# Performance work log

Hardware: AMD Instinct MI355X
Metric: run time of the kernel (lower is better)

Reference implementation:

```python
import jax, jax.numpy as jnp
import numpy as np

B, L, S, H, E, D = 2, 2048, 2048, 16, 64, 64


def setup_inputs() -> dict:
    key = jax.random.key(0)
    kq, kk, kv = jax.random.split(key, 3)
    queries = jax.random.normal(kq, (B, L, H, E), dtype=jnp.float32)
    keys = jax.random.normal(kk, (B, S, H, E), dtype=jnp.float32)
    values = jax.random.normal(kv, (B, S, H, D), dtype=jnp.float32)
    # causal mask: True = masked out (matches masked_fill semantics)
    causal = jnp.triu(jnp.ones((L, S), dtype=bool), k=1)
    attn_mask = jnp.broadcast_to(causal, (B, L, S))
    return {"queries": queries, "keys": keys, "values": values, "attn_mask": attn_mask}


def reference(queries, keys, values, attn_mask):
    # queries: [B,L,H,E], keys: [B,S,H,E], values: [B,S,H,D], attn_mask: [B,L,S] bool
    E_ = queries.shape[-1]
    scale = 1.0 / jnp.sqrt(jnp.asarray(E_, dtype=queries.dtype))
    scores = jnp.einsum('blhe,bshe->bhls', queries, keys)  # [B,H,L,S]
    scores = jnp.where(attn_mask[:, None, :, :], -jnp.inf, scores)
    A = jax.nn.softmax(scale * scores, axis=-1)
    A = jnp.nan_to_num(A)  # fully-masked rows -> 0 (dropout prob is 0.0)
    V = jnp.einsum('bhls,bshd->blhd', A, values)  # [B,L,H,D]
    return (V, A)
```

## Files before the change

kernel.cpp:

```cpp
#include <hip/hip_runtime.h>
#include <cstdint>
#include <cstddef>

#define B_ 2
#define L_ 2048
#define S_ 2048
#define H_ 16
#define E_ 64
#define D_ 64

#define LOG2E_SCALE 0.18033688011112042f

typedef __attribute__((ext_vector_type(8))) short short8;
typedef __attribute__((ext_vector_type(4))) float float4v;
typedef __attribute__((ext_vector_type(4))) unsigned short ushort4v;
typedef __attribute__((ext_vector_type(2))) unsigned int uint2v;

__device__ __forceinline__ unsigned short f2bf(float f) {
  unsigned u = __builtin_bit_cast(unsigned, f);
  u += 0x7FFFu + ((u >> 16) & 1u);
  return (unsigned short)(u >> 16);
}

__device__ __forceinline__ float myexp2(float x) {
#if __has_builtin(__builtin_amdgcn_exp2f)
  return __builtin_amdgcn_exp2f(x);
#else
  return exp2f(x);
#endif
}

__global__ __launch_bounds__(256)
void conv_nh_kernel(const float* __restrict__ in, unsigned short* __restrict__ out) {
  unsigned idx4 = blockIdx.x * 256u + threadIdx.x;
  unsigned e4 = idx4 & 15u;
  unsigned h  = (idx4 >> 4) & 15u;
  unsigned n  = (idx4 >> 8) & 2047u;
  unsigned b  = idx4 >> 19;
  float4v v = *(const float4v*)(in + (size_t)idx4 * 4u);
  ushort4v o;
  o.x = f2bf(v.x); o.y = f2bf(v.y); o.z = f2bf(v.z); o.w = f2bf(v.w);
  *(ushort4v*)(out + (((size_t)(b * H_ + h) * 2048u + n) * 16u + e4) * 4u) = o;
}

__global__ __launch_bounds__(256)
void conv_vt_kernel(const float* __restrict__ V, unsigned short* __restrict__ VT) {
  __shared__ float tile[64 * 65];
  const int st = blockIdx.x, h = blockIdx.y, b = blockIdx.z;
  const int tid = threadIdx.x;
  const float* vb = V + ((size_t)(b * S_ + st * 64) * H_ + h) * D_;
  #pragma unroll
  for (int i = 0; i < 4; ++i) {
    int e = tid + i * 256;
    int row = e >> 4, c4 = (e & 15) * 4;
    float4v v = *(const float4v*)(vb + (size_t)row * (H_ * D_) + c4);
    tile[row * 65 + c4 + 0] = v.x; tile[row * 65 + c4 + 1] = v.y;
    tile[row * 65 + c4 + 2] = v.z; tile[row * 65 + c4 + 3] = v.w;
  }
  __syncthreads();
  #pragma unroll
  for (int i = 0; i < 4; ++i) {
    int e = tid + i * 256;
    int d = e >> 4, c4 = (e & 15) * 4;
    ushort4v o;
    o.x = f2bf(tile[(c4 + 0) * 65 + d]); o.y = f2bf(tile[(c4 + 1) * 65 + d]);
    o.z = f2bf(tile[(c4 + 2) * 65 + d]); o.w = f2bf(tile[(c4 + 3) * 65 + d]);
    *(ushort4v*)(VT + ((size_t)(b * H_ + h) * D_ + d) * S_ + st * 64 + c4) = o;
  }
}

__global__ __launch_bounds__(256, 4)
void fullattn5_kernel(const unsigned short* __restrict__ Qbf,
                      const unsigned short* __restrict__ Kbf,
                      const unsigned short* __restrict__ VT,
                      float* __restrict__ OutV, float* __restrict__ OutA) {
  __shared__ alignas(16) char smem[18688];
  unsigned short* Ps = (unsigned short*)smem;
  float* Lbuf = (float*)(smem + 18432);
  float* Obuf = (float*)smem;

  const int tid = threadIdx.x;
  const int w = tid >> 6;
  const int lane = tid & 63;
  const int quad = lane >> 4;
  const int n16 = lane & 15;

  const int st = (int)(gridDim.x - 1u - blockIdx.x);
  const int h = blockIdx.y, b = blockIdx.z;
  const int l0 = st * 16;
  const int jt = st >> 2;
  const int doff = (st & 3) * 16;

  float* arow0 = OutA + ((size_t)((b * H_ + h) * L_) + l0) * (size_t)S_;

  {
    const int c4start = (jt + 1) * 16;
    #pragma unroll
    for (int i = 0; i < 4; ++i) {
      float4v* rp = (float4v*)(arow0 + (size_t)(w * 4 + i) * S_);
      for (int c4 = c4start + lane; c4 < S_ / 4; c4 += 64) {
        float4v z = {0.f, 0.f, 0.f, 0.f};
        __builtin_nontemporal_store(z, rp + c4);
      }
    }
  }

  const unsigned short* qrow = Qbf + ((size_t)(b * H_ + h) * L_ + l0 + n16) * E_;
  const short8 qB0 = *(const short8*)(qrow + quad * 8);
  const short8 qB1 = *(const short8*)(qrow + 32 + quad * 8);

  const unsigned short* kbase = Kbf + (size_t)(b * H_ + h) * S_ * E_;
  const unsigned short* vbase = VT + (size_t)(b * H_ + h) * D_ * S_;

  float lsum = 0.f;

  short8 kA0[4], kA1[4], kB0[4], kB1[4];
  auto loadK = [&](int j, short8 (&b0)[4], short8 (&b1)[4]) {
    const unsigned short* kb = kbase + (size_t)j * 64 * E_;
    #pragma unroll
    for (int t = 0; t < 4; ++t) {
      const unsigned short* kr = kb + (size_t)(t * 16 + n16) * E_;
      b0[t] = *(const short8*)(kr + quad * 8);
      b1[t] = *(const short8*)(kr + 32 + quad * 8);
    }
  };

  auto procK = [&](const short8 (&b0)[4], const short8 (&b1)[4], int j) {
    #pragma unroll
    for (int t = 0; t < 4; ++t) {
      float4v acc = {0.f, 0.f, 0.f, 0.f};
      acc = __builtin_amdgcn_mfma_f32_16x16x32_bf16(b0[t], qB0, acc, 0, 0, 0);
      acc = __builtin_amdgcn_mfma_f32_16x16x32_bf16(b1[t], qB1, acc, 0, 0, 0);
      #pragma unroll
      for (int r = 0; r < 4; ++r) {
        float x = acc[r] * LOG2E_SCALE;
        if (j == jt && (t * 16 + quad * 4 + r > doff + n16)) x = -__builtin_inff();
        lsum += myexp2(x);
      }
    }
  };

  if (w <= jt) {
    loadK(w, kA0, kA1);
    int j = w;
    for (;;) {
      if (j + 4 <= jt) loadK(j + 4, kB0, kB1);
      procK(kA0, kA1, j);
      j += 4;
      if (j > jt) break;
      if (j + 4 <= jt) loadK(j + 4, kA0, kA1);
      procK(kB0, kB1, j);
      j += 4;
      if (j > jt) break;
    }
  }

  lsum += __shfl_xor(lsum, 16);
  lsum += __shfl_xor(lsum, 32);
  if (quad == 0) Lbuf[w * 16 + n16] = lsum;
  __syncthreads();
  const float inv_l = 1.0f / (Lbuf[n16] + Lbuf[16 + n16] + Lbuf[32 + n16] + Lbuf[48 + n16]);

  float4v oacc[4];
  #pragma unroll
  for (int t2 = 0; t2 < 4; ++t2) oacc[t2] = (float4v){0.f, 0.f, 0.f, 0.f};

  float* arowL = arow0 + (size_t)n16 * S_ + quad * 4;

  int par = 0;
  for (int j = w; j <= jt; j += 4, par ^= 1) {
    short8 v0f[4], v1f[4];
    #pragma unroll
    for (int t2 = 0; t2 < 4; ++t2) {
      const unsigned short* vr = vbase + (size_t)(t2 * 16 + n16) * S_ + j * 64;
      v0f[t2] = *(const short8*)(vr + quad * 8);
      v1f[t2] = *(const short8*)(vr + 32 + quad * 8);
    }

    const unsigned short* kb = kbase + (size_t)j * 64 * E_;
    unsigned short* psw = Ps + (size_t)((w << 1) | par) * (16 * 72);
    #pragma unroll
    for (int t = 0; t < 4; ++t) {
      const unsigned short* kr = kb + (size_t)(t * 16 + n16) * E_;
      const short8 b0 = *(const short8*)(kr + quad * 8);
      const short8 b1 = *(const short8*)(kr + 32 + quad * 8);
      float4v acc = {0.f, 0.f, 0.f, 0.f};
      acc = __builtin_amdgcn_mfma_f32_16x16x32_bf16(b0, qB0, acc, 0, 0, 0);
      acc = __builtin_amdgcn_mfma_f32_16x16x32_bf16(b1, qB1, acc, 0, 0, 0);
      float p[4];
      #pragma unroll
      for (int r = 0; r < 4; ++r) {
        p[r] = myexp2(acc[r] * LOG2E_SCALE) * inv_l;
        if (j == jt && (t * 16 + quad * 4 + r > doff + n16)) p[r] = 0.f;
      }
      float4v p4 = {p[0], p[1], p[2], p[3]};
      __builtin_nontemporal_store(p4, (float4v*)(arowL + j * 64 + t * 16));
      uint2v dw;
      dw.x = (unsigned)f2bf(p[0]) | ((unsigned)f2bf(p[1]) << 16);
      dw.y = (unsigned)f2bf(p[2]) | ((unsigned)f2bf(p[3]) << 16);
      *(uint2v*)&psw[n16 * 72 + t * 16 + quad * 4] = dw;
    }
    __builtin_amdgcn_wave_barrier();
    const short8 aP0 = *(const short8*)&psw[n16 * 72 + quad * 8];
    const short8 aP1 = *(const short8*)&psw[n16 * 72 + 32 + quad * 8];
    #pragma unroll
    for (int t2 = 0; t2 < 4; ++t2) {
      oacc[t2] = __builtin_amdgcn_mfma_f32_16x16x32_bf16(aP0, v0f[t2], oacc[t2], 0, 0, 0);
      oacc[t2] = __builtin_amdgcn_mfma_f32_16x16x32_bf16(aP1, v1f[t2], oacc[t2], 0, 0, 0);
    }
  }

  __syncthreads();
  #pragma unroll
  for (int t2 = 0; t2 < 4; ++t2)
    #pragma unroll
    for (int r = 0; r < 4; ++r)
      Obuf[(size_t)(w * 16 + quad * 4 + r) * 68 + t2 * 16 + n16] = oacc[t2][r];
  __syncthreads();
  {
    const int row = tid >> 4;
    const int c0 = (tid & 15) * 4;
    float4v s = *(const float4v*)&Obuf[(size_t)row * 68 + c0];
    #pragma unroll
    for (int ww = 1; ww < 4; ++ww) {
      float4v t = *(const float4v*)&Obuf[(size_t)(ww * 16 + row) * 68 + c0];
      s.x += t.x; s.y += t.y; s.z += t.z; s.w += t.w;
    }
    float* op = OutV + ((size_t)(b * L_ + l0 + row) * H_ + h) * D_ + c0;
    __builtin_nontemporal_store(s, (float4v*)op);
  }
}

__global__ __launch_bounds__(256, 4)
void fullattn_fb_kernel(const float* __restrict__ Q, const float* __restrict__ K,
                        const float* __restrict__ V, float* __restrict__ OutV,
                        float* __restrict__ OutA) {
  __shared__ alignas(16) unsigned short Qs[64 * 72];
  __shared__ alignas(16) unsigned short Ks[64 * 72];
  __shared__ alignas(16) unsigned short VTs[64 * 72];
  __shared__ alignas(16) unsigned short Ps[64 * 72];
  const int tid = threadIdx.x;
  const int w = tid >> 6, lane = tid & 63, quad = lane >> 4, n16 = lane & 15;
  const int lt = (int)(gridDim.x - 1u - blockIdx.x);
  const int h = blockIdx.y, b = blockIdx.z;
  const int l0 = lt * 64;
  float* arow0 = OutA + ((size_t)((b * H_ + h) * L_) + l0) * (size_t)S_;
  {
    const int c4start = (lt + 1) * 16;
    for (int rr = w; rr < 64; rr += 4) {
      float4v* rp = (float4v*)(arow0 + (size_t)rr * S_);
      for (int c4 = c4start + lane; c4 < S_ / 4; c4 += 64) {
        float4v z = {0.f, 0.f, 0.f, 0.f};
        __builtin_nontemporal_store(z, rp + c4);
      }
    }
  }
  {
    const float* qb = Q + ((size_t)(b * L_ + l0) * H_ + h) * E_;
    #pragma unroll
    for (int i = 0; i < 4; ++i) {
      int e = tid + i * 256;
      int row = e >> 4, c4 = (e & 15) * 4;
      float4v qv = *(const float4v*)(qb + (size_t)row * (H_ * E_) + c4);
      ushort4v o; o.x = f2bf(qv.x); o.y = f2bf(qv.y); o.z = f2bf(qv.z); o.w = f2bf(qv.w);
      *(ushort4v*)&Qs[row * 72 + c4] = o;
    }
  }
  auto stageK = [&](int j) {
    const float* kb = K + ((size_t)(b * S_ + j * 64) * H_ + h) * E_;
    #pragma unroll
    for (int i = 0; i < 4; ++i) {
      int e = tid + i * 256;
      int row = e >> 4, c4 = (e & 15) * 4;
      float4v kv = *(const float4v*)(kb + (size_t)row * (H_ * E_) + c4);
      ushort4v o; o.x = f2bf(kv.x); o.y = f2bf(kv.y); o.z = f2bf(kv.z); o.w = f2bf(kv.w);
      *(ushort4v*)&Ks[row * 72 + c4] = o;
    }
  };
  auto stageV = [&](int j) {
    const float* vb = V + ((size_t)(b * S_ + j * 64) * H_ + h) * D_;
    const int d = lane;
    #pragma unroll
    for (int i = 0; i < 8; ++i) {
      int s2 = w * 8 + i;
      float f0 = vb[(size_t)(2 * s2) * (H_ * D_) + d];
      float f1 = vb[(size_t)(2 * s2 + 1) * (H_ * D_) + d];
      unsigned pk = (unsigned)f2bf(f0) | ((unsigned)f2bf(f1) << 16);
      *(unsigned*)&VTs[d * 72 + 2 * s2] = pk;
    }
  };
  __syncthreads();
  const short8 aQ0 = *(const short8*)&Qs[(w * 16 + n16) * 72 + quad * 8];
  const short8 aQ1 = *(const short8*)&Qs[(w * 16 + n16) * 72 + 32 + quad * 8];
  float m2[4], lsum[4];
  #pragma unroll
  for (int r = 0; r < 4; ++r) { m2[r] = -__builtin_inff(); lsum[r] = 0.f; }
  for (int j = 0; j <= lt; ++j) {
    stageK(j);
    __syncthreads();
    float x[4][4];
    #pragma unroll
    for (int t = 0; t < 4; ++t) {
      const short8 b0 = *(const short8*)&Ks[(t * 16 + n16) * 72 + quad * 8];
      const short8 b1 = *(const short8*)&Ks[(t * 16 + n16) * 72 + 32 + quad * 8];
      float4v acc = {0.f, 0.f, 0.f, 0.f};
      acc = __builtin_amdgcn_mfma_f32_16x16x32_bf16(aQ0, b0, acc, 0, 0, 0);
      acc = __builtin_amdgcn_mfma_f32_16x16x32_bf16(aQ1, b1, acc, 0, 0, 0);
      #pragma unroll
      for (int r = 0; r < 4; ++r) x[t][r] = acc[r] * LOG2E_SCALE;
    }
    if (j == lt) {
      #pragma unroll
      for (int t = 0; t < 4; ++t)
        #pragma unroll
        for (int r = 0; r < 4; ++r)
          if (t * 16 + n16 > w * 16 + quad * 4 + r) x[t][r] = -__builtin_inff();
    }
    #pragma unroll
    for (int r = 0; r < 4; ++r) {
      float mx = fmaxf(fmaxf(x[0][r], x[1][r]), fmaxf(x[2][r], x[3][r]));
      #pragma unroll
      for (int off = 8; off >= 1; off >>= 1) mx = fmaxf(mx, __shfl_xor(mx, off));
      float mnew = fmaxf(m2[r], mx);
      float alpha = myexp2(m2[r] - mnew);
      float sm = myexp2(x[0][r] - mnew) + myexp2(x[1][r] - mnew) +
                 myexp2(x[2][r] - mnew) + myexp2(x[3][r] - mnew);
      #pragma unroll
      for (int off = 8; off >= 1; off >>= 1) sm += __shfl_xor(sm, off);
      lsum[r] = lsum[r] * alpha + sm;
      m2[r] = mnew;
    }
    __syncthreads();
  }
  float inv_l[4];
  #pragma unroll
  for (int r = 0; r < 4; ++r) inv_l[r] = 1.0f / lsum[r];
  float4v oacc[4];
  #pragma unroll
  for (int t2 = 0; t2 < 4; ++t2) oacc[t2] = (float4v){0.f, 0.f, 0.f, 0.f};
  for (int j = 0; j <= lt; ++j) {
    stageK(j);
    stageV(j);
    __syncthreads();
    float* arow = arow0 + (size_t)(w * 16 + quad * 4) * S_ + j * 64 + n16;
    #pragma unroll
    for (int t = 0; t < 4; ++t) {
      const short8 b0 = *(const short8*)&Ks[(t * 16 + n16) * 72 + quad * 8];
      const short8 b1 = *(const short8*)&Ks[(t * 16 + n16) * 72 + 32 + quad * 8];
      float4v acc = {0.f, 0.f, 0.f, 0.f};
      acc = __builtin_amdgcn_mfma_f32_16x16x32_bf16(aQ0, b0, acc, 0, 0, 0);
      acc = __builtin_amdgcn_mfma_f32_16x16x32_bf16(aQ1, b1, acc, 0, 0, 0);
      #pragma unroll
      for (int r = 0; r < 4; ++r) {
        float p = myexp2(acc[r] * LOG2E_SCALE - m2[r]) * inv_l[r];
        if (j == lt && (t * 16 + n16 > w * 16 + quad * 4 + r)) p = 0.f;
        __builtin_nontemporal_store(p, arow + (size_t)r * S_ + t * 16);
        float pp = __shfl_xor(p, 1);
        unsigned short sp = f2bf(p), spp = f2bf(pp);
        unsigned dw = (n16 & 1) ? ((unsigned)spp | ((unsigned)sp << 16))
                                : ((unsigned)sp | ((unsigned)spp << 16));
        *(unsigned*)&Ps[(w * 16 + quad * 4 + r) * 72 + (t * 16 + (n16 & ~1))] = dw;
      }
    }
    __builtin_amdgcn_wave_barrier();
    const short8 aP0 = *(const short8*)&Ps[(w * 16 + n16) * 72 + quad * 8];
    const short8 aP1 = *(const short8*)&Ps[(w * 16 + n16) * 72 + 32 + quad * 8];
    #pragma unroll
    for (int t2 = 0; t2 < 4; ++t2) {
      const short8 v0 = *(const short8*)&VTs[(t2 * 16 + n16) * 72 + quad * 8];
      const short8 v1 = *(const short8*)&VTs[(t2 * 16 + n16) * 72 + 32 + quad * 8];
      oacc[t2] = __builtin_amdgcn_mfma_f32_16x16x32_bf16(aP0, v0, oacc[t2], 0, 0, 0);
      oacc[t2] = __builtin_amdgcn_mfma_f32_16x16x32_bf16(aP1, v1, oacc[t2], 0, 0, 0);
    }
    __syncthreads();
  }
  float* ob = OutV + ((size_t)(b * L_ + l0 + w * 16 + quad * 4) * H_ + h) * D_ + n16;
  #pragma unroll
  for (int t2 = 0; t2 < 4; ++t2)
    #pragma unroll
    for (int r = 0; r < 4; ++r)
      __builtin_nontemporal_store(oacc[t2][r], ob + (size_t)r * (H_ * D_) + t2 * 16);
}

extern "C" void kernel_launch(void* const* d_in, const int* in_sizes, int n_in,
                              void* d_out, int out_size, void* d_ws, size_t ws_size,
                              hipStream_t stream) {
  (void)in_sizes; (void)n_in; (void)out_size;
  const float* Q = (const float*)d_in[0];
  const float* K = (const float*)d_in[1];
  const float* V = (const float*)d_in[2];
  float* OutV = (float*)d_out;
  float* OutA = (float*)d_out + (size_t)B_ * L_ * H_ * D_;

  const size_t bytes_each = (size_t)B_ * H_ * 2048 * 64 * sizeof(unsigned short);
  if (ws_size >= 3 * bytes_each) {
    unsigned short* Qbf = (unsigned short*)d_ws;
    unsigned short* Kbf = (unsigned short*)((char*)d_ws + bytes_each);
    unsigned short* VTb = (unsigned short*)((char*)d_ws + 2 * bytes_each);
    const int nblk = (B_ * 2048 * H_ * E_ / 4) / 256;
    conv_nh_kernel<<<nblk, 256, 0, stream>>>(Q, Qbf);
    conv_nh_kernel<<<nblk, 256, 0, stream>>>(K, Kbf);
    conv_vt_kernel<<<dim3(S_ / 64, H_, B_), 256, 0, stream>>>(V, VTb);
    fullattn5_kernel<<<dim3(L_ / 16, H_, B_), 256, 0, stream>>>(Qbf, Kbf, VTb, OutV, OutA);
  } else {
    fullattn_fb_kernel<<<dim3(L_ / 64, H_, B_), 256, 0, stream>>>(Q, K, V, OutV, OutA);
  }
}
```

Baseline: 745.5 us.

## Software-pipeline PV pass across key tiles and merge Q/K conversion launches

The second attention pass is restructured so that the PV MFMAs for the previous tile are issued after loading the next K tile, and the V loads for the current tile come after them, overlapping global loads with matrix work. Probability stores to the A output are deferred until after the LDS round-trip. The separate Q and K bf16 conversion launches are merged into one kernel that picks its source by block parity, saving one launch. The pipelining adds register pressure under the 4-blocks-per-SM launch bound and may cause spills.

```diff
diff --git a/kernel.cpp b/kernel.cpp
--- a/kernel.cpp
+++ b/kernel.cpp
@@ -31,8 +31,12 @@
 }
 
 __global__ __launch_bounds__(256)
-void conv_nh_kernel(const float* __restrict__ in, unsigned short* __restrict__ out) {
-  unsigned idx4 = blockIdx.x * 256u + threadIdx.x;
+void conv_qk_kernel(const float* __restrict__ Qi, const float* __restrict__ Ki,
+                    unsigned short* __restrict__ Qo, unsigned short* __restrict__ Ko) {
+  const unsigned bx = blockIdx.x;
+  const float* in = (bx & 1u) ? Ki : Qi;
+  unsigned short* out = (bx & 1u) ? Ko : Qo;
+  unsigned idx4 = (bx >> 1) * 256u + threadIdx.x;
   unsigned e4 = idx4 & 15u;
   unsigned h  = (idx4 >> 4) & 15u;
   unsigned n  = (idx4 >> 8) & 2047u;
@@ -70,7 +74,7 @@
 }
 
 __global__ __launch_bounds__(256, 4)
-void fullattn5_kernel(const unsigned short* __restrict__ Qbf,
+void fullattn6_kernel(const unsigned short* __restrict__ Qbf,
                       const unsigned short* __restrict__ Kbf,
                       const unsigned short* __restrict__ VT,
                       float* __restrict__ OutV, float* __restrict__ OutA) {
@@ -113,45 +117,44 @@
   const unsigned short* vbase = VT + (size_t)(b * H_ + h) * D_ * S_;
 
   float lsum = 0.f;
-
-  short8 kA0[4], kA1[4], kB0[4], kB1[4];
-  auto loadK = [&](int j, short8 (&b0)[4], short8 (&b1)[4]) {
-    const unsigned short* kb = kbase + (size_t)j * 64 * E_;
-    #pragma unroll
-    for (int t = 0; t < 4; ++t) {
-      const unsigned short* kr = kb + (size_t)(t * 16 + n16) * E_;
-      b0[t] = *(const short8*)(kr + quad * 8);
-      b1[t] = *(const short8*)(kr + 32 + quad * 8);
-    }
-  };
-
-  auto procK = [&](const short8 (&b0)[4], const short8 (&b1)[4], int j) {
-    #pragma unroll
-    for (int t = 0; t < 4; ++t) {
-      float4v acc = {0.f, 0.f, 0.f, 0.f};
-      acc = __builtin_amdgcn_mfma_f32_16x16x32_bf16(b0[t], qB0, acc, 0, 0, 0);
-      acc = __builtin_amdgcn_mfma_f32_16x16x32_bf16(b1[t], qB1, acc, 0, 0, 0);
-      #pragma unroll
-      for (int r = 0; r < 4; ++r) {
-        float x = acc[r] * LOG2E_SCALE;
-        if (j == jt && (t * 16 + quad * 4 + r > doff + n16)) x = -__builtin_inff();
-        lsum += myexp2(x);
-      }
-    }
-  };
-
-  if (w <= jt) {
-    loadK(w, kA0, kA1);
-    int j = w;
-    for (;;) {
-      if (j + 4 <= jt) loadK(j + 4, kB0, kB1);
-      procK(kA0, kA1, j);
-      j += 4;
-      if (j > jt) break;
-      if (j + 4 <= jt) loadK(j + 4, kA0, kA1);
-      procK(kB0, kB1, j);
-      j += 4;
-      if (j > jt) break;
+  {
+    short8 kA0[4], kA1[4], kB0[4], kB1[4];
+    auto loadK = [&](int j, short8 (&b0)[4], short8 (&b1)[4]) {
+      const unsigned short* kb = kbase + (size_t)j * 64 * E_;
+      #pragma unroll
+      for (int t = 0; t < 4; ++t) {
+        const unsigned short* kr = kb + (size_t)(t * 16 + n16) * E_;
+        b0[t] = *(const short8*)(kr + quad * 8);
+        b1[t] = *(const short8*)(kr + 32 + quad * 8);
+      }
+    };
+    auto procK = [&](const short8 (&b0)[4], const short8 (&b1)[4], int j) {
+      #pragma unroll
+      for (int t = 0; t < 4; ++t) {
+        float4v acc = {0.f, 0.f, 0.f, 0.f};
+        acc = __builtin_amdgcn_mfma_f32_16x16x32_bf16(b0[t], qB0, acc, 0, 0, 0);
+        acc = __builtin_amdgcn_mfma_f32_16x16x32_bf16(b1[t], qB1, acc, 0, 0, 0);
+        #pragma unroll
+        for (int r = 0; r < 4; ++r) {
+          float x = acc[r] * LOG2E_SCALE;
+          if (j == jt && (t * 16 + quad * 4 + r > doff + n16)) x = -__builtin_inff();
+          lsum += myexp2(x);
+        }
+      }
+    };
+    if (w <= jt) {
+      loadK(w, kA0, kA1);
+      int j = w;
+      for (;;) {
+        if (j + 4 <= jt) loadK(j + 4, kB0, kB1);
+        procK(kA0, kA1, j);
+        j += 4;
+        if (j > jt) break;
+        if (j + 4 <= jt) loadK(j + 4, kA0, kA1);
+        procK(kB0, kB1, j);
+        j += 4;
+        if (j > jt) break;
+      }
     }
   }
 
@@ -167,47 +170,74 @@
 
   float* arowL = arow0 + (size_t)n16 * S_ + quad * 4;
 
-  int par = 0;
-  for (int j = w; j <= jt; j += 4, par ^= 1) {
-    short8 v0f[4], v1f[4];
+  short8 kc0[4], kc1[4];
+  short8 vf0[4], vf1[4];
+  short8 aP0, aP1;
+
+  auto loadK2 = [&](int j) {
+    const unsigned short* kb = kbase + (size_t)j * 64 * E_;
+    #pragma unroll
+    for (int t = 0; t < 4; ++t) {
+      const unsigned short* kr = kb + (size_t)(t * 16 + n16) * E_;
+      kc0[t] = *(const short8*)(kr + quad * 8);
+      kc1[t] = *(const short8*)(kr + 32 + quad * 8);
+    }
+  };
+  auto loadV2 = [&](int j) {
     #pragma unroll
     for (int t2 = 0; t2 < 4; ++t2) {
       const unsigned short* vr = vbase + (size_t)(t2 * 16 + n16) * S_ + j * 64;
-      v0f[t2] = *(const short8*)(vr + quad * 8);
-      v1f[t2] = *(const short8*)(vr + 32 + quad * 8);
-    }
-
-    const unsigned short* kb = kbase + (size_t)j * 64 * E_;
+      vf0[t2] = *(const short8*)(vr + quad * 8);
+      vf1[t2] = *(const short8*)(vr + 32 + quad * 8);
+    }
+  };
+  auto tailQK = [&](int j, int par) {
     unsigned short* psw = Ps + (size_t)((w << 1) | par) * (16 * 72);
+    float4v p4[4];
     #pragma unroll
     for (int t = 0; t < 4; ++t) {
-      const unsigned short* kr = kb + (size_t)(t * 16 + n16) * E_;
-      const short8 b0 = *(const short8*)(kr + quad * 8);
-      const short8 b1 = *(const short8*)(kr + 32 + quad * 8);
       float4v acc = {0.f, 0.f, 0.f, 0.f};
-      acc = __builtin_amdgcn_mfma_f32_16x16x32_bf16(b0, qB0, acc, 0, 0, 0);
-      acc = __builtin_amdgcn_mfma_f32_16x16x32_bf16(b1, qB1, acc, 0, 0, 0);
-      float p[4];
+      acc = __builtin_amdgcn_mfma_f32_16x16x32_bf16(kc0[t], qB0, acc, 0, 0, 0);
+      acc = __builtin_amdgcn_mfma_f32_16x16x32_bf16(kc1[t], qB1, acc, 0, 0, 0);
       #pragma unroll
       for (int r = 0; r < 4; ++r) {
-        p[r] = myexp2(acc[r] * LOG2E_SCALE) * inv_l;
-        if (j == jt && (t * 16 + quad * 4 + r > doff + n16)) p[r] = 0.f;
-      }
-      float4v p4 = {p[0], p[1], p[2], p[3]};
-      __builtin_nontemporal_store(p4, (float4v*)(arowL + j * 64 + t * 16));
+        float p = myexp2(acc[r] * LOG2E_SCALE) * inv_l;
+        if (j == jt && (t * 16 + quad * 4 + r > doff + n16)) p = 0.f;
+        p4[t][r] = p;
+      }
       uint2v dw;
-      dw.x = (unsigned)f2bf(p[0]) | ((unsigned)f2bf(p[1]) << 16);
-      dw.y = (unsigned)f2bf(p[2]) | ((unsigned)f2bf(p[3]) << 16);
+      dw.x = (unsigned)f2bf(p4[t][0]) | ((unsigned)f2bf(p4[t][1]) << 16);
+      dw.y = (unsigned)f2bf(p4[t][2]) | ((unsigned)f2bf(p4[t][3]) << 16);
       *(uint2v*)&psw[n16 * 72 + t * 16 + quad * 4] = dw;
     }
     __builtin_amdgcn_wave_barrier();
-    const short8 aP0 = *(const short8*)&psw[n16 * 72 + quad * 8];
-    const short8 aP1 = *(const short8*)&psw[n16 * 72 + 32 + quad * 8];
+    aP0 = *(const short8*)&psw[n16 * 72 + quad * 8];
+    aP1 = *(const short8*)&psw[n16 * 72 + 32 + quad * 8];
+    __builtin_amdgcn_wave_barrier();
+    #pragma unroll
+    for (int t = 0; t < 4; ++t)
+      __builtin_nontemporal_store(p4[t], (float4v*)(arowL + j * 64 + t * 16));
+  };
+  auto doPV = [&]() {
     #pragma unroll
     for (int t2 = 0; t2 < 4; ++t2) {
-      oacc[t2] = __builtin_amdgcn_mfma_f32_16x16x32_bf16(aP0, v0f[t2], oacc[t2], 0, 0, 0);
-      oacc[t2] = __builtin_amdgcn_mfma_f32_16x16x32_bf16(aP1, v1f[t2], oacc[t2], 0, 0, 0);
-    }
+      oacc[t2] = __builtin_amdgcn_mfma_f32_16x16x32_bf16(aP0, vf0[t2], oacc[t2], 0, 0, 0);
+      oacc[t2] = __builtin_amdgcn_mfma_f32_16x16x32_bf16(aP1, vf1[t2], oacc[t2], 0, 0, 0);
+    }
+  };
+
+  if (w <= jt) {
+    loadK2(w);
+    loadV2(w);
+    tailQK(w, 0);
+    int par = 1;
+    for (int j = w + 4; j <= jt; j += 4, par ^= 1) {
+      loadK2(j);
+      doPV();
+      loadV2(j);
+      tailQK(j, par);
+    }
+    doPV();
   }
 
   __syncthreads();
@@ -398,10 +428,9 @@
     unsigned short* Kbf = (unsigned short*)((char*)d_ws + bytes_each);
     unsigned short* VTb = (unsigned short*)((char*)d_ws + 2 * bytes_each);
     const int nblk = (B_ * 2048 * H_ * E_ / 4) / 256;
-    conv_nh_kernel<<<nblk, 256, 0, stream>>>(Q, Qbf);
-    conv_nh_kernel<<<nblk, 256, 0, stream>>>(K, Kbf);
+    conv_qk_kernel<<<2 * nblk, 256, 0, stream>>>(Q, K, Qbf, Kbf);
     conv_vt_kernel<<<dim3(S_ / 64, H_, B_), 256, 0, stream>>>(V, VTb);
-    fullattn5_kernel<<<dim3(L_ / 16, H_, B_), 256, 0, stream>>>(Qbf, Kbf, VTb, OutV, OutA);
+    fullattn6_kernel<<<dim3(L_ / 16, H_, B_), 256, 0, stream>>>(Qbf, Kbf, VTb, OutV, OutA);
   } else {
     fullattn_fb_kernel<<<dim3(L_ / 64, H_, B_), 256, 0, stream>>>(Q, K, V, OutV, OutA);
   }
```

After: 757.1 us. No clear change (+1.6%).

## Pair complementary causal row tiles per block and merge Q/K conversion launches

Applied to the files above, without the earlier changes.

Each attention block now handles two 16-row query tiles, st and 127-st, so every block does roughly the same amount of causal work. The grid shrinks from 128 to 64 tiles per head, which removes the tail imbalance of the descending-work schedule. The Q and K bf16 conversions are merged into one launch to save a kernel launch. The cost is fewer blocks in flight, serialized passes with extra syncthreads inside each block, and a slightly larger LDS footprint.

```diff
diff --git a/kernel.cpp b/kernel.cpp
--- a/kernel.cpp
+++ b/kernel.cpp
@@ -31,8 +31,12 @@
 }
 
 __global__ __launch_bounds__(256)
-void conv_nh_kernel(const float* __restrict__ in, unsigned short* __restrict__ out) {
-  unsigned idx4 = blockIdx.x * 256u + threadIdx.x;
+void conv_qk_kernel(const float* __restrict__ Qi, const float* __restrict__ Ki,
+                    unsigned short* __restrict__ Qo, unsigned short* __restrict__ Ko) {
+  const unsigned bx = blockIdx.x;
+  const float* in = (bx & 1u) ? Ki : Qi;
+  unsigned short* out = (bx & 1u) ? Ko : Qo;
+  unsigned idx4 = (bx >> 1) * 256u + threadIdx.x;
   unsigned e4 = idx4 & 15u;
   unsigned h  = (idx4 >> 4) & 15u;
   unsigned n  = (idx4 >> 8) & 2047u;
@@ -70,11 +74,11 @@
 }
 
 __global__ __launch_bounds__(256, 4)
-void fullattn5_kernel(const unsigned short* __restrict__ Qbf,
+void fullattn7_kernel(const unsigned short* __restrict__ Qbf,
                       const unsigned short* __restrict__ Kbf,
                       const unsigned short* __restrict__ VT,
                       float* __restrict__ OutV, float* __restrict__ OutA) {
-  __shared__ alignas(16) char smem[18688];
+  __shared__ alignas(16) char smem[18944];
   unsigned short* Ps = (unsigned short*)smem;
   float* Lbuf = (float*)(smem + 18432);
   float* Obuf = (float*)smem;
@@ -85,15 +89,19 @@
   const int quad = lane >> 4;
   const int n16 = lane & 15;
 
-  const int st = (int)(gridDim.x - 1u - blockIdx.x);
   const int h = blockIdx.y, b = blockIdx.z;
-  const int l0 = st * 16;
-  const int jt = st >> 2;
-  const int doff = (st & 3) * 16;
-
-  float* arow0 = OutA + ((size_t)((b * H_ + h) * L_) + l0) * (size_t)S_;
-
-  {
+  const int stA = (int)blockIdx.x;
+  const int stB = 127 - stA;
+  const int jtA = stA >> 2, doffA = (stA & 3) * 16;
+  const int jtB = stB >> 2, doffB = (stB & 3) * 16;
+
+  const unsigned short* kbase = Kbf + (size_t)(b * H_ + h) * S_ * E_;
+  const unsigned short* vbase = VT + (size_t)(b * H_ + h) * D_ * S_;
+
+  float* arowA = OutA + ((size_t)((b * H_ + h) * L_) + stA * 16) * (size_t)S_;
+  float* arowB = OutA + ((size_t)((b * H_ + h) * L_) + stB * 16) * (size_t)S_;
+
+  auto zfill = [&](float* arow0, int jt) {
     const int c4start = (jt + 1) * 16;
     #pragma unroll
     for (int i = 0; i < 4; ++i) {
@@ -103,121 +111,123 @@
         __builtin_nontemporal_store(z, rp + c4);
       }
     }
-  }
-
-  const unsigned short* qrow = Qbf + ((size_t)(b * H_ + h) * L_ + l0 + n16) * E_;
-  const short8 qB0 = *(const short8*)(qrow + quad * 8);
-  const short8 qB1 = *(const short8*)(qrow + 32 + quad * 8);
-
-  const unsigned short* kbase = Kbf + (size_t)(b * H_ + h) * S_ * E_;
-  const unsigned short* vbase = VT + (size_t)(b * H_ + h) * D_ * S_;
-
-  float lsum = 0.f;
-
-  short8 kA0[4], kA1[4], kB0[4], kB1[4];
-  auto loadK = [&](int j, short8 (&b0)[4], short8 (&b1)[4]) {
-    const unsigned short* kb = kbase + (size_t)j * 64 * E_;
-    #pragma unroll
-    for (int t = 0; t < 4; ++t) {
-      const unsigned short* kr = kb + (size_t)(t * 16 + n16) * E_;
-      b0[t] = *(const short8*)(kr + quad * 8);
-      b1[t] = *(const short8*)(kr + 32 + quad * 8);
-    }
-  };
-
-  auto procK = [&](const short8 (&b0)[4], const short8 (&b1)[4], int j) {
-    #pragma unroll
-    for (int t = 0; t < 4; ++t) {
-      float4v acc = {0.f, 0.f, 0.f, 0.f};
-      acc = __builtin_amdgcn_mfma_f32_16x16x32_bf16(b0[t], qB0, acc, 0, 0, 0);
-      acc = __builtin_amdgcn_mfma_f32_16x16x32_bf16(b1[t], qB1, acc, 0, 0, 0);
-      #pragma unroll
-      for (int r = 0; r < 4; ++r) {
-        float x = acc[r] * LOG2E_SCALE;
-        if (j == jt && (t * 16 + quad * 4 + r > doff + n16)) x = -__builtin_inff();
-        lsum += myexp2(x);
-      }
-    }
-  };
-
-  if (w <= jt) {
-    loadK(w, kA0, kA1);
-    int j = w;
-    for (;;) {
-      if (j + 4 <= jt) loadK(j + 4, kB0, kB1);
-      procK(kA0, kA1, j);
-      j += 4;
-      if (j > jt) break;
-      if (j + 4 <= jt) loadK(j + 4, kA0, kA1);
-      procK(kB0, kB1, j);
-      j += 4;
-      if (j > jt) break;
-    }
-  }
-
-  lsum += __shfl_xor(lsum, 16);
-  lsum += __shfl_xor(lsum, 32);
-  if (quad == 0) Lbuf[w * 16 + n16] = lsum;
+  };
+  zfill(arowA, jtA);
+  zfill(arowB, jtB);
+
+  const unsigned short* qrowA = Qbf + ((size_t)(b * H_ + h) * L_ + stA * 16 + n16) * E_;
+  const short8 qA0 = *(const short8*)(qrowA + quad * 8);
+  const short8 qA1 = *(const short8*)(qrowA + 32 + quad * 8);
+  const unsigned short* qrowB = Qbf + ((size_t)(b * H_ + h) * L_ + stB * 16 + n16) * E_;
+  const short8 qB0 = *(const short8*)(qrowB + quad * 8);
+  const short8 qB1 = *(const short8*)(qrowB + 32 + quad * 8);
+
+  auto pass1 = [&](int jt, int doff, short8 q0, short8 q1) -> float {
+    float ls = 0.f;
+    short8 kA0[4], kA1[4], kB0[4], kB1[4];
+    auto loadK = [&](int j, short8 (&c0)[4], short8 (&c1)[4]) {
+      const unsigned short* kb = kbase + (size_t)j * 64 * E_;
+      #pragma unroll
+      for (int t = 0; t < 4; ++t) {
+        const unsigned short* kr = kb + (size_t)(t * 16 + n16) * E_;
+        c0[t] = *(const short8*)(kr + quad * 8);
+        c1[t] = *(const short8*)(kr + 32 + quad * 8);
+      }
+    };
+    auto procK = [&](const short8 (&c0)[4], const short8 (&c1)[4], int j) {
+      #pragma unroll
+      for (int t = 0; t < 4; ++t) {
+        float4v acc = {0.f, 0.f, 0.f, 0.f};
+        acc = __builtin_amdgcn_mfma_f32_16x16x32_bf16(c0[t], q0, acc, 0, 0, 0);
+        acc = __builtin_amdgcn_mfma_f32_16x16x32_bf16(c1[t], q1, acc, 0, 0, 0);
+        #pragma unroll
+        for (int r = 0; r < 4; ++r) {
+          float x = acc[r] * LOG2E_SCALE;
+          if (j == jt && (t * 16 + quad * 4 + r > doff + n16)) x = -__builtin_inff();
+          ls += myexp2(x);
+        }
+      }
+    };
+    if (w <= jt) {
+      loadK(w, kA0, kA1);
+      int j = w;
+      for (;;) {
+        if (j + 4 <= jt) loadK(j + 4, kB0, kB1);
+        procK(kA0, kA1, j);
+        j += 4;
+        if (j > jt) break;
+        if (j + 4 <= jt) loadK(j + 4, kA0, kA1);
+        procK(kB0, kB1, j);
+        j += 4;
+        if (j > jt) break;
+      }
+    }
+    return ls;
+  };
+
+  float lsA = pass1(jtA, doffA, qA0, qA1);
+  float lsB = pass1(jtB, doffB, qB0, qB1);
+  lsA += __shfl_xor(lsA, 16); lsA += __shfl_xor(lsA, 32);
+  lsB += __shfl_xor(lsB, 16); lsB += __shfl_xor(lsB, 32);
+  if (quad == 0) { Lbuf[w * 16 + n16] = lsA; Lbuf[64 + w * 16 + n16] = lsB; }
   __syncthreads();
-  const float inv_l = 1.0f / (Lbuf[n16] + Lbuf[16 + n16] + Lbuf[32 + n16] + Lbuf[48 + n16]);
-
-  float4v oacc[4];
-  #pragma unroll
-  for (int t2 = 0; t2 < 4; ++t2) oacc[t2] = (float4v){0.f, 0.f, 0.f, 0.f};
-
-  float* arowL = arow0 + (size_t)n16 * S_ + quad * 4;
-
-  int par = 0;
-  for (int j = w; j <= jt; j += 4, par ^= 1) {
-    short8 v0f[4], v1f[4];
-    #pragma unroll
-    for (int t2 = 0; t2 < 4; ++t2) {
-      const unsigned short* vr = vbase + (size_t)(t2 * 16 + n16) * S_ + j * 64;
-      v0f[t2] = *(const short8*)(vr + quad * 8);
-      v1f[t2] = *(const short8*)(vr + 32 + quad * 8);
-    }
-
-    const unsigned short* kb = kbase + (size_t)j * 64 * E_;
-    unsigned short* psw = Ps + (size_t)((w << 1) | par) * (16 * 72);
-    #pragma unroll
-    for (int t = 0; t < 4; ++t) {
-      const unsigned short* kr = kb + (size_t)(t * 16 + n16) * E_;
-      const short8 b0 = *(const short8*)(kr + quad * 8);
-      const short8 b1 = *(const short8*)(kr + 32 + quad * 8);
-      float4v acc = {0.f, 0.f, 0.f, 0.f};
-      acc = __builtin_amdgcn_mfma_f32_16x16x32_bf16(b0, qB0, acc, 0, 0, 0);
-      acc = __builtin_amdgcn_mfma_f32_16x16x32_bf16(b1, qB1, acc, 0, 0, 0);
-      float p[4];
-      #pragma unroll
-      for (int r = 0; r < 4; ++r) {
-        p[r] = myexp2(acc[r] * LOG2E_SCALE) * inv_l;
-        if (j == jt && (t * 16 + quad * 4 + r > doff + n16)) p[r] = 0.f;
-      }
-      float4v p4 = {p[0], p[1], p[2], p[3]};
-      __builtin_nontemporal_store(p4, (float4v*)(arowL + j * 64 + t * 16));
-      uint2v dw;
-      dw.x = (unsigned)f2bf(p[0]) | ((unsigned)f2bf(p[1]) << 16);
-      dw.y = (unsigned)f2bf(p[2]) | ((unsigned)f2bf(p[3]) << 16);
-      *(uint2v*)&psw[n16 * 72 + t * 16 + quad * 4] = dw;
-    }
-    __builtin_amdgcn_wave_barrier();
-    const short8 aP0 = *(const short8*)&psw[n16 * 72 + quad * 8];
-    const short8 aP1 = *(const short8*)&psw[n16 * 72 + 32 + quad * 8];
-    #pragma unroll
-    for (int t2 = 0; t2 < 4; ++t2) {
-      oacc[t2] = __builtin_amdgcn_mfma_f32_16x16x32_bf16(aP0, v0f[t2], oacc[t2], 0, 0, 0);
-      oacc[t2] = __builtin_amdgcn_mfma_f32_16x16x32_bf16(aP1, v1f[t2], oacc[t2], 0, 0, 0);
-    }
-  }
-
-  __syncthreads();
-  #pragma unroll
-  for (int t2 = 0; t2 < 4; ++t2)
-    #pragma unroll
-    for (int r = 0; r < 4; ++r)
-      Obuf[(size_t)(w * 16 + quad * 4 + r) * 68 + t2 * 16 + n16] = oacc[t2][r];
-  __syncthreads();
-  {
+  const float invA = 1.0f / (Lbuf[n16] + Lbuf[16 + n16] + Lbuf[32 + n16] + Lbuf[48 + n16]);
+  const float invB = 1.0f / (Lbuf[64 + n16] + Lbuf[80 + n16] + Lbuf[96 + n16] + Lbuf[112 + n16]);
+
+  auto pass2 = [&](int jt, int doff, short8 q0, short8 q1, float inv_l,
+                   float* arow0, float4v (&oacc)[4]) {
+    float* arowL = arow0 + (size_t)n16 * S_ + quad * 4;
+    int par = 0;
+    for (int j = w; j <= jt; j += 4, par ^= 1) {
+      short8 v0f[4], v1f[4];
+      #pragma unroll
+      for (int t2 = 0; t2 < 4; ++t2) {
+        const unsigned short* vr = vbase + (size_t)(t2 * 16 + n16) * S_ + j * 64;
+        v0f[t2] = *(const short8*)(vr + quad * 8);
+        v1f[t2] = *(const short8*)(vr + 32 + quad * 8);
+      }
+      const unsigned short* kb = kbase + (size_t)j * 64 * E_;
+      unsigned short* psw = Ps + (size_t)((w << 1) | par) * (16 * 72);
+      #pragma unroll
+      for (int t = 0; t < 4; ++t) {
+        const unsigned short* kr = kb + (size_t)(t * 16 + n16) * E_;
+        const short8 c0 = *(const short8*)(kr + quad * 8);
+        const short8 c1 = *(const short8*)(kr + 32 + quad * 8);
+        float4v acc = {0.f, 0.f, 0.f, 0.f};
+        acc = __builtin_amdgcn_mfma_f32_16x16x32_bf16(c0, q0, acc, 0, 0, 0);
+        acc = __builtin_amdgcn_mfma_f32_16x16x32_bf16(c1, q1, acc, 0, 0, 0);
+        float p[4];
+        #pragma unroll
+        for (int r = 0; r < 4; ++r) {
+          p[r] = myexp2(acc[r] * LOG2E_SCALE) * inv_l;
+          if (j == jt && (t * 16 + quad * 4 + r > doff + n16)) p[r] = 0.f;
+        }
+        float4v p4 = {p[0], p[1], p[2], p[3]};
+        __builtin_nontemporal_store(p4, (float4v*)(arowL + j * 64 + t * 16));
+        uint2v dw;
+        dw.x = (unsigned)f2bf(p[0]) | ((unsigned)f2bf(p[1]) << 16);
+        dw.y = (unsigned)f2bf(p[2]) | ((unsigned)f2bf(p[3]) << 16);
+        *(uint2v*)&psw[n16 * 72 + t * 16 + quad * 4] = dw;
+      }
+      __builtin_amdgcn_wave_barrier();
+      const short8 aP0 = *(const short8*)&psw[n16 * 72 + quad * 8];
+      const short8 aP1 = *(const short8*)&psw[n16 * 72 + 32 + quad * 8];
+      #pragma unroll
+      for (int t2 = 0; t2 < 4; ++t2) {
+        oacc[t2] = __builtin_amdgcn_mfma_f32_16x16x32_bf16(aP0, v0f[t2], oacc[t2], 0, 0, 0);
+        oacc[t2] = __builtin_amdgcn_mfma_f32_16x16x32_bf16(aP1, v1f[t2], oacc[t2], 0, 0, 0);
+      }
+    }
+  };
+
+  auto combineO = [&](int l0, float4v (&oacc)[4]) {
+    __syncthreads();
+    #pragma unroll
+    for (int t2 = 0; t2 < 4; ++t2)
+      #pragma unroll
+      for (int r = 0; r < 4; ++r)
+        Obuf[(size_t)(w * 16 + quad * 4 + r) * 68 + t2 * 16 + n16] = oacc[t2][r];
+    __syncthreads();
     const int row = tid >> 4;
     const int c0 = (tid & 15) * 4;
     float4v s = *(const float4v*)&Obuf[(size_t)row * 68 + c0];
@@ -228,7 +238,19 @@
     }
     float* op = OutV + ((size_t)(b * L_ + l0 + row) * H_ + h) * D_ + c0;
     __builtin_nontemporal_store(s, (float4v*)op);
-  }
+    __syncthreads();
+  };
+
+  float4v oacc[4];
+  #pragma unroll
+  for (int t2 = 0; t2 < 4; ++t2) oacc[t2] = (float4v){0.f, 0.f, 0.f, 0.f};
+  pass2(jtA, doffA, qA0, qA1, invA, arowA, oacc);
+  combineO(stA * 16, oacc);
+
+  #pragma unroll
+  for (int t2 = 0; t2 < 4; ++t2) oacc[t2] = (float4v){0.f, 0.f, 0.f, 0.f};
+  pass2(jtB, doffB, qB0, qB1, invB, arowB, oacc);
+  combineO(stB * 16, oacc);
 }
 
 __global__ __launch_bounds__(256, 4)
@@ -398,10 +420,9 @@
     unsigned short* Kbf = (unsigned short*)((char*)d_ws + bytes_each);
     unsigned short* VTb = (unsigned short*)((char*)d_ws + 2 * bytes_each);
     const int nblk = (B_ * 2048 * H_ * E_ / 4) / 256;
-    conv_nh_kernel<<<nblk, 256, 0, stream>>>(Q, Qbf);
-    conv_nh_kernel<<<nblk, 256, 0, stream>>>(K, Kbf);
+    conv_qk_kernel<<<2 * nblk, 256, 0, stream>>>(Q, K, Qbf, Kbf);
     conv_vt_kernel<<<dim3(S_ / 64, H_, B_), 256, 0, stream>>>(V, VTb);
-    fullattn5_kernel<<<dim3(L_ / 16, H_, B_), 256, 0, stream>>>(Qbf, Kbf, VTb, OutV, OutA);
+    fullattn7_kernel<<<dim3(64, H_, B_), 256, 0, stream>>>(Qbf, Kbf, VTb, OutV, OutA);
   } else {
     fullattn_fb_kernel<<<dim3(L_ / 64, H_, B_), 256, 0, stream>>>(Q, K, V, OutV, OutA);
   }
```

New measurement: 698.4 us, median of 2. 6.3% less time.
